# Kernel optimization log

Measured on AMD Instinct MI355X. Metric: run time of the kernel, lower is better.

Reference implementation:

```python
import jax, jax.numpy as jnp
import numpy as np

D_MODEL = 1024
D_FF = 4096
NUM_EXPERTS = 8
TOP_K = 2  # expert_capacity


def setup_inputs() -> dict:
    key = jax.random.key(0)
    ks = jax.random.split(key, 7)
    s_in = 1.0 / np.sqrt(D_MODEL)
    s_ff = 1.0 / np.sqrt(D_FF)
    x = jax.random.normal(ks[0], (2, 2048, D_MODEL), dtype=jnp.float32)
    gate_w = jax.random.uniform(ks[1], (NUM_EXPERTS, D_MODEL), jnp.float32, -s_in, s_in)
    gate_b = jax.random.uniform(ks[2], (NUM_EXPERTS,), jnp.float32, -s_in, s_in)
    w1 = jax.random.uniform(ks[3], (NUM_EXPERTS, D_MODEL, D_FF), jnp.float32, -s_in, s_in)
    b1 = jax.random.uniform(ks[4], (NUM_EXPERTS, D_FF), jnp.float32, -s_in, s_in)
    w2 = jax.random.uniform(ks[5], (NUM_EXPERTS, D_FF, D_MODEL), jnp.float32, -s_ff, s_ff)
    b2 = jax.random.uniform(ks[6], (NUM_EXPERTS, D_MODEL), jnp.float32, -s_ff, s_ff)
    return {"x": x, "gate_w": gate_w, "gate_b": gate_b,
            "w1": w1, "b1": b1, "w2": w2, "b2": b2}


def reference(x, gate_w, gate_b, w1, b1, w2, b2):
    E = gate_w.shape[0]
    # Router
    logits = jnp.einsum('bsd,ed->bse', x, gate_w) + gate_b  # [B,S,E]
    top_vals, top_idx = jax.lax.top_k(logits, TOP_K)        # [B,S,K]
    top_w = jax.nn.softmax(top_vals, axis=-1)               # softmax over the top-k logits
    probs = jax.nn.softmax(logits, axis=-1)
    usage = probs.mean(axis=(0, 1))                         # [E]
    load_balancing_loss = E * jnp.sum(usage ** 2) - 1.0
    # Combine weights: sum over top-k slots of weight * one_hot(expert)
    combine = jnp.sum(top_w[..., None] * jax.nn.one_hot(top_idx, E, dtype=x.dtype), axis=2)  # [B,S,E]
    # All experts over all tokens (faithful to the naive dense-then-mask module)
    h = jax.nn.gelu(jnp.einsum('bsd,edf->ebsf', x, w1) + b1[:, None, None, :], approximate=False)
    expert_out = jnp.einsum('ebsf,efd->ebsd', h, w2) + b2[:, None, None, :]  # [E,B,S,D]
    output = jnp.einsum('bse,ebsd->bsd', combine, expert_out)
    return output, load_balancing_loss
```

## Files before the change

### kernel.cpp

```cpp
#include <hip/hip_runtime.h>
#include <hip/hip_bf16.h>
#include <math.h>


#define D_MODEL 1024
#define D_FF    4096
#define NE      8
#define NTOK    4096
#define CAP     4096

typedef __attribute__((ext_vector_type(4))) float f32x4;
typedef __attribute__((ext_vector_type(8))) short s16x8;

__device__ __forceinline__ short f2bf(float f) {
    union { float f; unsigned u; } v; v.f = f;
    unsigned r = v.u + 0x7FFFu + ((v.u >> 16) & 1u);
    return (short)(r >> 16);
}

__device__ __forceinline__ float gelu_f(float x) {
    float u = x * x;
    float v = __builtin_fmaf(0.044715f, u, 1.0f);
    float y2 = 1.5957691216057308f * x * v;
    float r = __builtin_amdgcn_rcpf(__expf(y2) + 1.0f);
    return x - x * r;
}

__device__ __forceinline__ void gload16(const void* g, void* l) {
    __builtin_amdgcn_global_load_lds(
        (const __attribute__((address_space(1))) unsigned*)g,
        (__attribute__((address_space(3))) unsigned*)l, 16, 0, 0);
}

__global__ __launch_bounds__(256) void router_kernel(
    const float* __restrict__ x, const float* __restrict__ gw,
    const float* __restrict__ gb,
    float* __restrict__ usage, int* __restrict__ eidx, float* __restrict__ wgt)
{
    __shared__ float s_gw[NE][D_MODEL];
    __shared__ float s_usage[NE];
    int tid = threadIdx.x;
    for (int i = tid * 4; i < NE * D_MODEL; i += 256 * 4)
        *(f32x4*)&s_gw[0][i] = *(const f32x4*)(gw + i);
    if (tid < NE) s_usage[tid] = 0.f;
    __syncthreads();

    int wid = tid >> 6, lane = tid & 63;
    int wave_stride = gridDim.x * 4;
    float l_usage[NE];
#pragma unroll
    for (int e = 0; e < NE; e++) l_usage[e] = 0.f;

    for (int t = blockIdx.x * 4 + wid; t < NTOK; t += wave_stride) {
        const float* xr = x + (size_t)t * D_MODEL;
        float acc[NE];
#pragma unroll
        for (int e = 0; e < NE; e++) acc[e] = 0.f;
        for (int i = lane * 4; i < D_MODEL; i += 64 * 4) {
            f32x4 xv = *(const f32x4*)(xr + i);
#pragma unroll
            for (int e = 0; e < NE; e++) {
                f32x4 gv = *(const f32x4*)&s_gw[e][i];
                acc[e] += xv[0]*gv[0] + xv[1]*gv[1] + xv[2]*gv[2] + xv[3]*gv[3];
            }
        }
#pragma unroll
        for (int e = 0; e < NE; e++) {
            float a = acc[e];
            for (int off = 32; off; off >>= 1) a += __shfl_down(a, off);
            acc[e] = a;
        }
        if (lane == 0) {
            float logits[NE];
            float mx = -1e30f;
#pragma unroll
            for (int e = 0; e < NE; e++) { logits[e] = acc[e] + gb[e]; mx = fmaxf(mx, logits[e]); }
            float se = 0.f;
            float pe[NE];
#pragma unroll
            for (int e = 0; e < NE; e++) { pe[e] = expf(logits[e] - mx); se += pe[e]; }
            float inv = 1.f / se;
#pragma unroll
            for (int e = 0; e < NE; e++) l_usage[e] += pe[e] * inv;
            int i0 = 0;
#pragma unroll
            for (int e = 1; e < NE; e++) if (logits[e] > logits[i0]) i0 = e;
            int i1 = -1;
#pragma unroll
            for (int e = 0; e < NE; e++) {
                if (e == i0) continue;
                if (i1 < 0 || logits[e] > logits[i1]) i1 = e;
            }
            float w0 = 1.f / (1.f + expf(logits[i1] - logits[i0]));
            eidx[t] = i0 | (i1 << 8);
            wgt[t] = w0;
        }
    }
    if (lane == 0) {
#pragma unroll
        for (int e = 0; e < NE; e++) atomicAdd(&s_usage[e], l_usage[e]);
    }
    __syncthreads();
    if (tid < NE) atomicAdd(&usage[tid], s_usage[tid]);
}

__global__ __launch_bounds__(256) void build_lists(
    const int* __restrict__ eidx, const float* __restrict__ wgt,
    int* __restrict__ cnt, int* __restrict__ tok_list, float* __restrict__ wt_list,
    int* __restrict__ tok2slot, float* __restrict__ wgt_p)
{
    int e = blockIdx.x;
    __shared__ int s_cnt;
    if (threadIdx.x == 0) s_cnt = 0;
    __syncthreads();
    for (int t = threadIdx.x; t < NTOK; t += 256) {
        int p = eidx[t];
        float w0 = wgt[t];
        if (e == 0) wgt_p[t] = w0;
        if ((p & 255) == e) {
            int s = atomicAdd(&s_cnt, 1);
            tok_list[e * CAP + s] = t; wt_list[e * CAP + s] = w0;
            tok2slot[2 * t] = (e << 16) | s;
        }
        if ((p >> 8) == e) {
            int s = atomicAdd(&s_cnt, 1);
            tok_list[e * CAP + s] = t; wt_list[e * CAP + s] = 1.f - w0;
            tok2slot[2 * t + 1] = (e << 16) | s;
        }
    }
    __syncthreads();
    if (threadIdx.x == 0) cnt[e] = s_cnt;
}

__global__ void compute_offsets(const int* __restrict__ cnt, int* __restrict__ offsets)
{
    int o = 0;
    for (int e = 0; e < NE; e++) { offsets[e] = o; o += cnt[e]; }
}

__global__ void write_loss(const float* __restrict__ usage, float* __restrict__ out_loss)
{
    float s = 0.f;
    for (int e = 0; e < NE; e++) { float u = usage[e] / (float)NTOK; s += u * u; }
    *out_loss = (float)NE * s - 1.f;
}

__global__ __launch_bounds__(256) void cvt_x_kernel(
    const float* __restrict__ x, short* __restrict__ xb)
{
    int i = (blockIdx.x * 256 + threadIdx.x) * 8;
    f32x4 a = *(const f32x4*)(x + i);
    f32x4 b = *(const f32x4*)(x + i + 4);
    s16x8 r;
    r[0]=f2bf(a[0]); r[1]=f2bf(a[1]); r[2]=f2bf(a[2]); r[3]=f2bf(a[3]);
    r[4]=f2bf(b[0]); r[5]=f2bf(b[1]); r[6]=f2bf(b[2]); r[7]=f2bf(b[3]);
    *(s16x8*)(xb + i) = r;
}

__global__ __launch_bounds__(256) void transpose_cvt(
    const float* __restrict__ src, short* __restrict__ dst, int R, int C)
{
    __shared__ float tile[64][65];
    int e = blockIdx.z;
    src += (size_t)e * R * C;
    dst += (size_t)e * R * C;
    int c0 = blockIdx.x * 64, r0 = blockIdx.y * 64;
    int tid = threadIdx.x;
    int lr = tid >> 2, lc = (tid & 3) * 16;

    const float* s = src + (size_t)(r0 + lr) * C + c0 + lc;
#pragma unroll
    for (int j = 0; j < 4; j++)
        *(f32x4*)&tile[lr][lc + j * 4] = *(const f32x4*)(s + j * 4);
    __syncthreads();

    short* d = dst + (size_t)(c0 + lr) * R + r0 + lc;
    s16x8 v0, v1;
#pragma unroll
    for (int j = 0; j < 8; j++) v0[j] = f2bf(tile[lc + j][lr]);
#pragma unroll
    for (int j = 0; j < 8; j++) v1[j] = f2bf(tile[lc + 8 + j][lr]);
    *(s16x8*)d = v0;
    *(s16x8*)(d + 8) = v1;
}

#define GEMM_STAGE(AS, BS, KT)                       \
    gload16(asrc0 + (KT), &AS[wid * 16][0]);         \
    gload16(asrc1 + (KT), &AS[64 + wid * 16][0]);    \
    gload16(bsrc0 + (KT), &BS[wid * 16][0]);         \
    gload16(bsrc1 + (KT), &BS[64 + wid * 16][0]);

#define GEMM_COMPUTE(AS, BS)                                                   \
    {                                                                          \
        s16x8 a[4], b[4];                                                      \
        int cidx = (kgr ^ ((lrow >> 1) & 3)) * 8;                              \
        _Pragma("unroll")                                                      \
        for (int i = 0; i < 4; i++) {                                          \
            a[i] = *(const s16x8*)&AS[wr * 64 + i * 16 + lrow][cidx];          \
            b[i] = *(const s16x8*)&BS[wc * 64 + i * 16 + lrow][cidx];          \
        }                                                                      \
        _Pragma("unroll")                                                      \
        for (int i = 0; i < 4; i++)                                            \
            _Pragma("unroll")                                                  \
            for (int j = 0; j < 4; j++)                                        \
                acc[i][j] = __builtin_amdgcn_mfma_f32_16x16x32_bf16(           \
                    a[i], b[j], acc[i][j], 0, 0, 0);                           \
    }

__global__ __launch_bounds__(256) void gemm1_kernel(
    const short* __restrict__ XB, const short* __restrict__ W1T,
    const float* __restrict__ b1, const int* __restrict__ cnt,
    const int* __restrict__ offsets, const int* __restrict__ tok_list,
    short* __restrict__ H)
{
    int r = blockIdx.x;
    int s = (r & 7) * 1024 + (r >> 3);
    int bx = s & 31;
    int by = s >> 5;
    int e  = by >> 5;
    int tm = by & 31;
    int ce = cnt[e];
    if (tm * 128 >= ce) return;
    int n0 = bx * 128;

    __shared__ __align__(16) short As[128][32];
    __shared__ __align__(16) short Bs[128][32];

    int tid = threadIdx.x;
    int lane = tid & 63, wid = tid >> 6;
    int wr = wid >> 1, wc = wid & 1;
    int lrow = lane & 15, kgr = lane >> 4;

    int srow = wid * 16 + (lane >> 2);
    int scol = ((lane & 3) ^ ((lane >> 3) & 3)) * 8;
    int am0 = tm * 128 + srow, am1 = am0 + 64;
    int tok0 = tok_list[e * CAP + (am0 < ce ? am0 : 0)];
    int tok1 = tok_list[e * CAP + (am1 < ce ? am1 : 0)];
    const short* asrc0 = XB + (size_t)tok0 * D_MODEL + scol;
    const short* asrc1 = XB + (size_t)tok1 * D_MODEL + scol;
    const short* bsrc0 = W1T + ((size_t)e * D_FF + n0 + srow) * D_MODEL + scol;
    const short* bsrc1 = bsrc0 + (size_t)64 * D_MODEL;

    f32x4 acc[4][4] = {};
    for (int kt = 0; kt < D_MODEL; kt += 32) {
        GEMM_STAGE(As, Bs, kt);
        __syncthreads();
        GEMM_COMPUTE(As, Bs);
        __syncthreads();
    }

    int offe = offsets[e];
    float bn[4];
#pragma unroll
    for (int j = 0; j < 4; j++) bn[j] = b1[e * D_FF + n0 + wc * 64 + j * 16 + lrow];
#pragma unroll
    for (int i = 0; i < 4; i++) {
#pragma unroll
        for (int q = 0; q < 4; q++) {
            int m = tm * 128 + wr * 64 + i * 16 + kgr * 4 + q;
            if (m >= ce) continue;
            short* hrow = H + (size_t)(offe + m) * D_FF;
#pragma unroll
            for (int j = 0; j < 4; j++) {
                int n = n0 + wc * 64 + j * 16 + lrow;
                hrow[n] = f2bf(gelu_f(acc[i][j][q] + bn[j]));
            }
        }
    }
}

__global__ __launch_bounds__(256) void gemm2_y_kernel(
    const short* __restrict__ H, const short* __restrict__ W2T,
    const float* __restrict__ b2, const int* __restrict__ cnt,
    const int* __restrict__ offsets, float* __restrict__ Y)
{
    int r = blockIdx.x;
    int s = (r & 7) * 256 + (r >> 3);
    int bx = s & 7;
    int by = s >> 3;
    int e  = by >> 5;
    int tm = by & 31;
    int ce = cnt[e];
    if (tm * 128 >= ce) return;
    int offe = offsets[e];
    int n0 = bx * 128;

    __shared__ __align__(16) short As[128][32];
    __shared__ __align__(16) short Bs[128][32];

    int tid = threadIdx.x;
    int lane = tid & 63, wid = tid >> 6;
    int wr = wid >> 1, wc = wid & 1;
    int lrow = lane & 15, kgr = lane >> 4;

    int srow = wid * 16 + (lane >> 2);
    int scol = ((lane & 3) ^ ((lane >> 3) & 3)) * 8;
    int am0 = tm * 128 + srow, am1 = am0 + 64;
    const short* asrc0 = H + (size_t)(offe + (am0 < ce ? am0 : 0)) * D_FF + scol;
    const short* asrc1 = H + (size_t)(offe + (am1 < ce ? am1 : 0)) * D_FF + scol;
    const short* bsrc0 = W2T + ((size_t)e * D_MODEL + n0 + srow) * D_FF + scol;
    const short* bsrc1 = bsrc0 + (size_t)64 * D_FF;

    f32x4 acc[4][4] = {};
    for (int kt = 0; kt < D_FF; kt += 32) {
        GEMM_STAGE(As, Bs, kt);
        __syncthreads();
        GEMM_COMPUTE(As, Bs);
        __syncthreads();
    }

    float bn[4];
#pragma unroll
    for (int j = 0; j < 4; j++) bn[j] = b2[e * D_MODEL + n0 + wc * 64 + j * 16 + lrow];
#pragma unroll
    for (int i = 0; i < 4; i++) {
#pragma unroll
        for (int q = 0; q < 4; q++) {
            int m = tm * 128 + wr * 64 + i * 16 + kgr * 4 + q;
            if (m >= ce) continue;
            float* yrow = Y + (size_t)(offe + m) * D_MODEL;
#pragma unroll
            for (int j = 0; j < 4; j++) {
                int n = n0 + wc * 64 + j * 16 + lrow;
                yrow[n] = acc[i][j][q] + bn[j];
            }
        }
    }
}

__global__ __launch_bounds__(256) void combine_kernel(
    const float* __restrict__ Y, const int* __restrict__ tok2slot,
    const float* __restrict__ wgt_p, const int* __restrict__ offsets,
    float* __restrict__ out)
{
    int t = blockIdx.x;
    int d = threadIdx.x * 4;
    int p0 = tok2slot[2 * t], p1 = tok2slot[2 * t + 1];
    int s0 = offsets[p0 >> 16] + (p0 & 0xFFFF);
    int s1 = offsets[p1 >> 16] + (p1 & 0xFFFF);
    float w0 = wgt_p[t], w1 = 1.f - w0;
    f32x4 a = *(const f32x4*)(Y + (size_t)s0 * D_MODEL + d);
    f32x4 b = *(const f32x4*)(Y + (size_t)s1 * D_MODEL + d);
    f32x4 r;
#pragma unroll
    for (int j = 0; j < 4; j++) r[j] = w0 * a[j] + w1 * b[j];
    *(f32x4*)(out + (size_t)t * D_MODEL + d) = r;
}

__global__ __launch_bounds__(256) void gemm2_kernel(
    const short* __restrict__ H, const short* __restrict__ W2T,
    const float* __restrict__ b2, const int* __restrict__ cnt,
    const int* __restrict__ offsets, const int* __restrict__ tok_list,
    const float* __restrict__ wt_list, float* __restrict__ out)
{
    int e  = blockIdx.y >> 5;
    int tm = blockIdx.y & 31;
    int ce = cnt[e];
    if (tm * 128 >= ce) return;
    int offe = offsets[e];
    int n0 = blockIdx.x * 128;
    int kz = blockIdx.z;
    const int KSPAN = D_FF / 2;
    int kbase = kz * KSPAN;

    __shared__ __align__(16) short As[128][32];
    __shared__ __align__(16) short Bs[128][32];

    int tid = threadIdx.x;
    int lane = tid & 63, wid = tid >> 6;
    int wr = wid >> 1, wc = wid & 1;
    int lrow = lane & 15, kgr = lane >> 4;

    int srow = wid * 16 + (lane >> 2);
    int scol = ((lane & 3) ^ ((lane >> 3) & 3)) * 8;
    int am0 = tm * 128 + srow, am1 = am0 + 64;
    const short* asrc0 = H + (size_t)(offe + (am0 < ce ? am0 : 0)) * D_FF + kbase + scol;
    const short* asrc1 = H + (size_t)(offe + (am1 < ce ? am1 : 0)) * D_FF + kbase + scol;
    const short* bsrc0 = W2T + ((size_t)e * D_MODEL + n0 + srow) * D_FF + kbase + scol;
    const short* bsrc1 = bsrc0 + (size_t)64 * D_FF;

    f32x4 acc[4][4] = {};
    for (int kt = 0; kt < KSPAN; kt += 32) {
        GEMM_STAGE(As, Bs, kt);
        __syncthreads();
        GEMM_COMPUTE(As, Bs);
        __syncthreads();
    }

    float bn[4];
#pragma unroll
    for (int j = 0; j < 4; j++)
        bn[j] = (kz == 0) ? b2[e * D_MODEL + n0 + wc * 64 + j * 16 + lrow] : 0.f;
#pragma unroll
    for (int i = 0; i < 4; i++) {
#pragma unroll
        for (int q = 0; q < 4; q++) {
            int m = tm * 128 + wr * 64 + i * 16 + kgr * 4 + q;
            if (m >= ce) continue;
            int tokm = tok_list[e * CAP + m];
            float wt = wt_list[e * CAP + m];
            float* orow = out + (size_t)tokm * D_MODEL;
#pragma unroll
            for (int j = 0; j < 4; j++) {
                int n = n0 + wc * 64 + j * 16 + lrow;
                atomicAdd(&orow[n], wt * (acc[i][j][q] + bn[j]));
            }
        }
    }
}

extern "C" void kernel_launch(void* const* d_in, const int* in_sizes, int n_in,
                              void* d_out, int out_size, void* d_ws, size_t ws_size,
                              hipStream_t stream)
{
    const float* x  = (const float*)d_in[0];
    const float* gw = (const float*)d_in[1];
    const float* gb = (const float*)d_in[2];
    const float* w1 = (const float*)d_in[3];
    const float* b1 = (const float*)d_in[4];
    const float* w2 = (const float*)d_in[5];
    const float* b2 = (const float*)d_in[6];
    float* out = (float*)d_out;

    char* w = (char*)d_ws;
    int*   cnt      = (int*)(w + 0);
    float* usage    = (float*)(w + 32);
    int*   offsets  = (int*)(w + 64);
    int*   tok_list = (int*)(w + 128);
    float* wt_list  = (float*)(w + 128 + 131072);
    int*   tok2slot = (int*)(w + 128 + 262144);
    float* wgt_p    = (float*)(w + 128 + 262144 + 32768);
    short* WT       = (short*)(w + 311424);
    short* H        = (short*)(w + 311424 + 67108864ull);
    float* Y        = (float*)(w + 311424 + 2ull * 67108864ull);
    size_t need_y   = 311424 + 2ull * 67108864ull + 33554432ull;
    bool   use_y    = ws_size >= need_y;
    int*   eidx     = (int*)WT;
    float* wgt      = (float*)(WT + NTOK * 2);
    short* XB       = (short*)d_out;

    hipMemsetAsync(d_ws, 0, 128, stream);

    router_kernel<<<256, 256, 0, stream>>>(x, gw, gb, usage, eidx, wgt);
    build_lists<<<NE, 256, 0, stream>>>(eidx, wgt, cnt, tok_list, wt_list, tok2slot, wgt_p);
    compute_offsets<<<1, 1, 0, stream>>>(cnt, offsets);
    cvt_x_kernel<<<NTOK * D_MODEL / (256 * 8), 256, 0, stream>>>(x, XB);

    transpose_cvt<<<dim3(D_FF / 64, D_MODEL / 64, NE), 256, 0, stream>>>(w1, WT, D_MODEL, D_FF);
    gemm1_kernel<<<(D_FF / 128) * NE * (CAP / 128), 256, 0, stream>>>(
        XB, WT, b1, cnt, offsets, tok_list, H);

    transpose_cvt<<<dim3(D_MODEL / 64, D_FF / 64, NE), 256, 0, stream>>>(w2, WT, D_FF, D_MODEL);

    if (use_y) {
        write_loss<<<1, 1, 0, stream>>>(usage, out + (size_t)NTOK * D_MODEL);
        gemm2_y_kernel<<<(D_MODEL / 128) * NE * (CAP / 128), 256, 0, stream>>>(
            H, WT, b2, cnt, offsets, Y);
        combine_kernel<<<NTOK, 256, 0, stream>>>(Y, tok2slot, wgt_p, offsets, out);
    } else {
        hipMemsetAsync(d_out, 0, (size_t)out_size * sizeof(float), stream);
        write_loss<<<1, 1, 0, stream>>>(usage, out + (size_t)NTOK * D_MODEL);
        gemm2_kernel<<<dim3(D_MODEL / 128, NE * (CAP / 128), 2), 256, 0, stream>>>(
            H, WT, b2, cnt, offsets, tok_list, wt_list, out);
    }
}
```

Baseline: 346.1 us.

## Double-buffer LDS tiles in expert GEMM k-loops to overlap loads with MFMA

The shared-memory A/B tiles in all three expert GEMM kernels become two-stage buffers. A shared k-loop macro prefetches the next k-slice into the alternate buffer while MFMAs run on the current one, leaving one barrier per iteration instead of two. The aim is to hide global-to-LDS load latency behind compute. The cost is twice the LDS per block, which can lower occupancy. Correctness depends on the asynchronous loads being complete before the barrier that precedes their use.

```diff
diff --git a/kernel.cpp b/kernel.cpp
--- a/kernel.cpp
+++ b/kernel.cpp
@@ -184,20 +184,20 @@
     *(s16x8*)(d + 8) = v1;
 }
 
-#define GEMM_STAGE(AS, BS, KT)                       \
-    gload16(asrc0 + (KT), &AS[wid * 16][0]);         \
-    gload16(asrc1 + (KT), &AS[64 + wid * 16][0]);    \
-    gload16(bsrc0 + (KT), &BS[wid * 16][0]);         \
-    gload16(bsrc1 + (KT), &BS[64 + wid * 16][0]);
-
-#define GEMM_COMPUTE(AS, BS)                                                   \
+#define GEMM_STAGE(BUF, KT)                               \
+    gload16(asrc0 + (KT), &As[BUF][wid * 16][0]);         \
+    gload16(asrc1 + (KT), &As[BUF][64 + wid * 16][0]);    \
+    gload16(bsrc0 + (KT), &Bs[BUF][wid * 16][0]);         \
+    gload16(bsrc1 + (KT), &Bs[BUF][64 + wid * 16][0]);
+
+#define GEMM_COMPUTE(BUF)                                                      \
     {                                                                          \
         s16x8 a[4], b[4];                                                      \
         int cidx = (kgr ^ ((lrow >> 1) & 3)) * 8;                              \
         _Pragma("unroll")                                                      \
         for (int i = 0; i < 4; i++) {                                          \
-            a[i] = *(const s16x8*)&AS[wr * 64 + i * 16 + lrow][cidx];          \
-            b[i] = *(const s16x8*)&BS[wc * 64 + i * 16 + lrow][cidx];          \
+            a[i] = *(const s16x8*)&As[BUF][wr * 64 + i * 16 + lrow][cidx];     \
+            b[i] = *(const s16x8*)&Bs[BUF][wc * 64 + i * 16 + lrow][cidx];     \
         }                                                                      \
         _Pragma("unroll")                                                      \
         for (int i = 0; i < 4; i++)                                            \
@@ -206,6 +206,18 @@
                 acc[i][j] = __builtin_amdgcn_mfma_f32_16x16x32_bf16(           \
                     a[i], b[j], acc[i][j], 0, 0, 0);                           \
     }
+
+#define GEMM_KLOOP(KTOT)                         \
+    GEMM_STAGE(0, 0);                            \
+    __syncthreads();                             \
+    int cur = 0;                                 \
+    for (int kt = 32; kt < (KTOT); kt += 32) {   \
+        GEMM_STAGE(cur ^ 1, kt);                 \
+        GEMM_COMPUTE(cur);                       \
+        __syncthreads();                         \
+        cur ^= 1;                                \
+    }                                            \
+    GEMM_COMPUTE(cur);
 
 __global__ __launch_bounds__(256) void gemm1_kernel(
     const short* __restrict__ XB, const short* __restrict__ W1T,
@@ -223,8 +235,8 @@
     if (tm * 128 >= ce) return;
     int n0 = bx * 128;
 
-    __shared__ __align__(16) short As[128][32];
-    __shared__ __align__(16) short Bs[128][32];
+    __shared__ __align__(16) short As[2][128][32];
+    __shared__ __align__(16) short Bs[2][128][32];
 
     int tid = threadIdx.x;
     int lane = tid & 63, wid = tid >> 6;
@@ -242,12 +254,7 @@
     const short* bsrc1 = bsrc0 + (size_t)64 * D_MODEL;
 
     f32x4 acc[4][4] = {};
-    for (int kt = 0; kt < D_MODEL; kt += 32) {
-        GEMM_STAGE(As, Bs, kt);
-        __syncthreads();
-        GEMM_COMPUTE(As, Bs);
-        __syncthreads();
-    }
+    GEMM_KLOOP(D_MODEL);
 
     int offe = offsets[e];
     float bn[4];
@@ -285,8 +292,8 @@
     int offe = offsets[e];
     int n0 = bx * 128;
 
-    __shared__ __align__(16) short As[128][32];
-    __shared__ __align__(16) short Bs[128][32];
+    __shared__ __align__(16) short As[2][128][32];
+    __shared__ __align__(16) short Bs[2][128][32];
 
     int tid = threadIdx.x;
     int lane = tid & 63, wid = tid >> 6;
@@ -302,12 +309,7 @@
     const short* bsrc1 = bsrc0 + (size_t)64 * D_FF;
 
     f32x4 acc[4][4] = {};
-    for (int kt = 0; kt < D_FF; kt += 32) {
-        GEMM_STAGE(As, Bs, kt);
-        __syncthreads();
-        GEMM_COMPUTE(As, Bs);
-        __syncthreads();
-    }
+    GEMM_KLOOP(D_FF);
 
     float bn[4];
 #pragma unroll
@@ -363,8 +365,8 @@
     const int KSPAN = D_FF / 2;
     int kbase = kz * KSPAN;
 
-    __shared__ __align__(16) short As[128][32];
-    __shared__ __align__(16) short Bs[128][32];
+    __shared__ __align__(16) short As[2][128][32];
+    __shared__ __align__(16) short Bs[2][128][32];
 
     int tid = threadIdx.x;
     int lane = tid & 63, wid = tid >> 6;
@@ -380,12 +382,7 @@
     const short* bsrc1 = bsrc0 + (size_t)64 * D_FF;
 
     f32x4 acc[4][4] = {};
-    for (int kt = 0; kt < KSPAN; kt += 32) {
-        GEMM_STAGE(As, Bs, kt);
-        __syncthreads();
-        GEMM_COMPUTE(As, Bs);
-        __syncthreads();
-    }
+    GEMM_KLOOP(KSPAN);
 
     float bn[4];
 #pragma unroll
@@ -454,8 +451,7 @@
 
     if (use_y) {
         write_loss<<<1, 1, 0, stream>>>(usage, out + (size_t)NTOK * D_MODEL);
-        gemm2_y_kernel<<<(D_MODEL / 128) * NE * (CAP / 128), 256, 0, stream>>>(
-            H, WT, b2, cnt, offsets, Y);
+        gemm2_y_kernel<<<2048, 256, 0, stream>>>(H, WT, b2, cnt, offsets, Y);
         combine_kernel<<<NTOK, 256, 0, stream>>>(Y, tok2slot, wgt_p, offsets, out);
     } else {
         hipMemsetAsync(d_out, 0, (size_t)out_size * sizeof(float), stream);
```

Measured after the change: 386.9 us. 11.8% more time.
